# Performance work log

Measured on AMD Instinct MI355X. Metric: run time of the kernel, lower is better.

## Reference

```python
import jax, jax.numpy as jnp
import numpy as np

N, E, G, T = 4096, 16384, 128, 100
DIMS = [(5, 64), (64, 128), (128, 256)]
EPS = 1e-5


def setup_inputs() -> dict:
    key = jax.random.key(0)
    ks = iter(jax.random.split(key, 64))
    d = {}
    d["x"] = jax.random.normal(next(ks), (N, 5), jnp.float32)
    d["edge_index"] = jax.random.randint(next(ks), (2, E), 0, N, jnp.int64)
    d["edge_attr"] = jax.random.uniform(next(ks), (E, 3), jnp.float32)
    d["batch_seg"] = jnp.sort(jax.random.randint(next(ks), (N,), 0, G, jnp.int64))
    for l, (cin, cout) in enumerate(DIMS, start=1):
        d[f"l{l}_W1"] = jax.random.normal(next(ks), (3, 32), jnp.float32) * 0.3
        d[f"l{l}_b1"] = jnp.zeros((32,), jnp.float32)
        d[f"l{l}_W2"] = jax.random.normal(next(ks), (32, cin * cout), jnp.float32) * 0.05
        d[f"l{l}_b2"] = jnp.zeros((cin * cout,), jnp.float32)
        d[f"l{l}_root"] = jax.random.normal(next(ks), (cin, cout), jnp.float32) * 0.1
        d[f"l{l}_bias"] = jnp.zeros((cout,), jnp.float32)
        d[f"bn{l}_g"] = jnp.ones((cout,), jnp.float32)
        d[f"bn{l}_b"] = jnp.zeros((cout,), jnp.float32)
        d[f"bn{l}_m"] = jax.random.normal(next(ks), (cout,), jnp.float32) * 0.01
        d[f"bn{l}_v"] = jax.random.uniform(next(ks), (cout,), jnp.float32, 0.5, 1.5)
    d["mlp_W"] = jax.random.normal(next(ks), (256, T), jnp.float32) * 0.06
    d["mlp_b"] = jnp.zeros((T,), jnp.float32)
    return d


def _nnconv(h, src, dst, edge_attr, W1, b1, W2, b2, root, bias, cin, cout):
    # edge MLP -> per-edge weight matrix [E, cin, cout]
    ew = (jax.nn.relu(edge_attr @ W1 + b1) @ W2 + b2).reshape(-1, cin, cout)
    msg = jnp.einsum('ei,eio->eo', h[src], ew)  # gather + per-edge matmul
    ssum = jax.ops.segment_sum(msg, dst, num_segments=N)
    cnt = jax.ops.segment_sum(jnp.ones((msg.shape[0],), msg.dtype), dst, num_segments=N)
    agg = ssum / jnp.maximum(cnt, 1.0)[:, None]  # scatter-mean
    return h @ root + agg + bias


def _bn(h, g, b, m, v):
    return g * (h - m) * jax.lax.rsqrt(v + EPS) + b


def reference(x, edge_index, edge_attr, batch_seg,
              l1_W1, l1_b1, l1_W2, l1_b2, l1_root, l1_bias, bn1_g, bn1_b, bn1_m, bn1_v,
              l2_W1, l2_b1, l2_W2, l2_b2, l2_root, l2_bias, bn2_g, bn2_b, bn2_m, bn2_v,
              l3_W1, l3_b1, l3_W2, l3_b2, l3_root, l3_bias, bn3_g, bn3_b, bn3_m, bn3_v,
              mlp_W, mlp_b):
    src, dst = edge_index[0], edge_index[1]
    h = _nnconv(x, src, dst, edge_attr, l1_W1, l1_b1, l1_W2, l1_b2, l1_root, l1_bias, 5, 64)
    h = jax.nn.relu(_bn(h, bn1_g, bn1_b, bn1_m, bn1_v))
    h = _nnconv(h, src, dst, edge_attr, l2_W1, l2_b1, l2_W2, l2_b2, l2_root, l2_bias, 64, 128)
    h = jax.nn.relu(_bn(h, bn2_g, bn2_b, bn2_m, bn2_v))
    h = _nnconv(h, src, dst, edge_attr, l3_W1, l3_b1, l3_W2, l3_b2, l3_root, l3_bias, 128, 256)
    h = jax.nn.relu(_bn(h, bn3_g, bn3_b, bn3_m, bn3_v))
    # global mean pool over graphs
    psum = jax.ops.segment_sum(h, batch_seg, num_segments=G)
    pcnt = jax.ops.segment_sum(jnp.ones((N,), h.dtype), batch_seg, num_segments=G)
    pooled = psum / jnp.maximum(pcnt, 1.0)[:, None]
    out = pooled @ mlp_W + mlp_b
    return jnp.where(out > 0, out, 0.1 * out)  # LeakyReLU(0.1)
```

## Files before the change

### kernel.cpp

```cpp
#include <hip/hip_runtime.h>
#include <cstdint>
#include <cstddef>

#define BN_EPS 1e-5f

typedef short bf16x8 __attribute__((ext_vector_type(8)));
typedef float f32x4  __attribute__((ext_vector_type(4)));
typedef unsigned short u16x8 __attribute__((ext_vector_type(8)));

__device__ __forceinline__ uint16_t f2bf_rte(float f) {
  uint32_t u = __float_as_uint(f);
  uint32_t r = u + 0x7fffu + ((u >> 16) & 1u);
  return (uint16_t)(r >> 16);
}
__device__ __forceinline__ float bf2f(uint16_t h) {
  return __uint_as_float(((uint32_t)h) << 16);
}
__device__ __forceinline__ void split_bf(float v, uint16_t& hi, uint16_t& lo) {
  hi = f2bf_rte(v);
  lo = f2bf_rte(v - bf2f(hi));
}

__global__ void zero_i32_k(int* p, int n) {
  int i = blockIdx.x * blockDim.x + threadIdx.x;
  if (i < n) p[i] = 0;
}

__global__ void hist_k(const int* __restrict__ dst, int* __restrict__ cnt, int E) {
  int e = blockIdx.x * blockDim.x + threadIdx.x;
  if (e < E) atomicAdd(&cnt[dst[e]], 1);
}

__global__ __launch_bounds__(1024) void scan_k(const int* __restrict__ cnt,
                                               int* __restrict__ offsets,
                                               int* __restrict__ cursor,
                                               int N, int total) {
  __shared__ int part[1024];
  int t = threadIdx.x;
  int a0 = cnt[4*t+0], a1 = cnt[4*t+1], a2 = cnt[4*t+2], a3 = cnt[4*t+3];
  part[t] = a0 + a1 + a2 + a3;
  __syncthreads();
  for (int off = 1; off < 1024; off <<= 1) {
    int v = (t >= off) ? part[t - off] : 0;
    __syncthreads();
    part[t] += v;
    __syncthreads();
  }
  int excl = (t == 0) ? 0 : part[t-1];
  int o0 = excl, o1 = o0 + a0, o2 = o1 + a1, o3 = o2 + a2;
  offsets[4*t+0] = o0; offsets[4*t+1] = o1; offsets[4*t+2] = o2; offsets[4*t+3] = o3;
  cursor [4*t+0] = o0; cursor [4*t+1] = o1; cursor [4*t+2] = o2; cursor [4*t+3] = o3;
  if (t == 0) offsets[N] = total;
}

__global__ void scatter_k(const int* __restrict__ dst, int* __restrict__ cursor,
                          int* __restrict__ csr, int E) {
  int e = blockIdx.x * blockDim.x + threadIdx.x;
  if (e < E) {
    int d = dst[e];
    int pos = atomicAdd(&cursor[d], 1);
    csr[pos] = e;
  }
}

__global__ void build_W2pT_k(const float* __restrict__ W2, const float* __restrict__ b2,
                             const float* __restrict__ root,
                             uint16_t* __restrict__ Bhi, uint16_t* __restrict__ Blo,
                             int cin, int cout, int Kpad) {
  int idx = blockIdx.x * blockDim.x + threadIdx.x;
  int total = cout * Kpad;
  if (idx >= total) return;
  int o  = idx / Kpad;
  int ki = idx - o * Kpad;
  float v = 0.f;
  if (ki < 34 * cin) {
    int k = ki / cin;
    int i = ki - k * cin;
    if (k < 32)       v = W2[(size_t)k * cin * cout + (size_t)i * cout + o];
    else if (k == 32) v = b2[(size_t)i * cout + o];
    else              v = root[(size_t)i * cout + o];
  }
  uint16_t hi, lo;
  split_bf(v, hi, lo);
  Bhi[idx] = hi;
  Blo[idx] = lo;
}

template<int CIN>
__global__ __launch_bounds__(256) void build_S_vec_k(const float* __restrict__ h,
                                                     const float* __restrict__ ea,
                                                     const float* __restrict__ W1,
                                                     const float* __restrict__ b1,
                                                     const int* __restrict__ src,
                                                     const int* __restrict__ csr,
                                                     const int* __restrict__ offsets,
                                                     uint16_t* __restrict__ Shi,
                                                     uint16_t* __restrict__ Slo,
                                                     int Kpad) {
  constexpr int CH = 8;
  constexpr int K1 = 33 * CIN;
  constexpr int NCH = K1 / 8;
  constexpr int NP = (NCH + 255) / 256;
  __shared__ float hs[CH][CIN];
  __shared__ float zs[CH][33];
  __shared__ int   es[CH];
  const int n = blockIdx.x;
  const int tid = threadIdx.x;
  const int base = offsets[n];
  const int deg  = offsets[n+1] - base;
  const float scale = 1.f / fmaxf((float)deg, 1.f);
  float acc[NP][8];
#pragma unroll
  for (int p = 0; p < NP; p++)
#pragma unroll
    for (int j = 0; j < 8; j++) acc[p][j] = 0.f;

  for (int c0 = 0; c0 < deg; c0 += CH) {
    const int cc = min(CH, deg - c0);
    if (tid < cc) es[tid] = csr[base + c0 + tid];
    __syncthreads();
    for (int idx = tid; idx < cc * CIN; idx += 256) {
      int slot = idx / CIN, i = idx - slot * CIN;
      hs[slot][i] = h[(size_t)src[es[slot]] * CIN + i];
    }
    for (int idx = tid; idx < cc * 33; idx += 256) {
      int slot = idx / 33, k = idx - slot * 33;
      float v;
      if (k == 32) v = 1.f;
      else {
        int e = es[slot];
        v = fmaxf(ea[e*3+0] * W1[k] + ea[e*3+1] * W1[32 + k] + ea[e*3+2] * W1[64 + k] + b1[k], 0.f);
      }
      zs[slot][k] = v;
    }
    __syncthreads();
#pragma unroll
    for (int p = 0; p < NP; p++) {
      int ch = p * 256 + tid;
      if (ch < NCH) {
        int ki0 = ch * 8;
        int k  = ki0 / CIN;
        int i0 = ki0 & (CIN - 1);
        for (int c = 0; c < cc; c++) {
          float zv = zs[c][k];
          float4 h0 = *(const float4*)&hs[c][i0];
          float4 h1 = *(const float4*)&hs[c][i0 + 4];
          acc[p][0] += zv * h0.x; acc[p][1] += zv * h0.y;
          acc[p][2] += zv * h0.z; acc[p][3] += zv * h0.w;
          acc[p][4] += zv * h1.x; acc[p][5] += zv * h1.y;
          acc[p][6] += zv * h1.z; acc[p][7] += zv * h1.w;
        }
      }
    }
    __syncthreads();
  }
  const size_t rowb = (size_t)n * Kpad;
#pragma unroll
  for (int p = 0; p < NP; p++) {
    int ch = p * 256 + tid;
    if (ch < NCH) {
      u16x8 hv, lv;
#pragma unroll
      for (int j = 0; j < 8; j++) {
        uint16_t hi, lo;
        split_bf(acc[p][j] * scale, hi, lo);
        hv[j] = hi; lv[j] = lo;
      }
      *(u16x8*)(Shi + rowb + ch * 8) = hv;
      *(u16x8*)(Slo + rowb + ch * 8) = lv;
    }
  }
  for (int c = tid; c < CIN / 8; c += 256) {
    int i0 = c * 8;
    float4 a = *(const float4*)&h[(size_t)n * CIN + i0];
    float4 b = *(const float4*)&h[(size_t)n * CIN + i0 + 4];
    float vals[8] = {a.x, a.y, a.z, a.w, b.x, b.y, b.z, b.w};
    u16x8 hv, lv;
#pragma unroll
    for (int j = 0; j < 8; j++) {
      uint16_t hi, lo;
      split_bf(vals[j], hi, lo);
      hv[j] = hi; lv[j] = lo;
    }
    *(u16x8*)(Shi + rowb + K1 + i0) = hv;
    *(u16x8*)(Slo + rowb + K1 + i0) = lv;
  }
  for (int ki = 34 * CIN + tid; ki < Kpad; ki += 256) {
    Shi[rowb + ki] = 0;
    Slo[rowb + ki] = 0;
  }
}

__global__ __launch_bounds__(256) void build_S5_k(const float* __restrict__ h,
                                                  const float* __restrict__ ea,
                                                  const float* __restrict__ W1,
                                                  const float* __restrict__ b1,
                                                  const int* __restrict__ src,
                                                  const int* __restrict__ csr,
                                                  const int* __restrict__ offsets,
                                                  uint16_t* __restrict__ Shi,
                                                  uint16_t* __restrict__ Slo,
                                                  int Kpad) {
  constexpr int CIN = 5, CH = 8;
  constexpr int K1 = 33 * CIN;
  constexpr int KT = 34 * CIN;
  __shared__ float hs[CH][CIN];
  __shared__ float zs[CH][33];
  __shared__ int   es[CH];
  const int n = blockIdx.x;
  const int tid = threadIdx.x;
  const int base = offsets[n];
  const int deg  = offsets[n+1] - base;
  const float scale = 1.f / fmaxf((float)deg, 1.f);
  float acc = 0.f;

  for (int c0 = 0; c0 < deg; c0 += CH) {
    const int cc = min(CH, deg - c0);
    if (tid < cc) es[tid] = csr[base + c0 + tid];
    __syncthreads();
    for (int idx = tid; idx < cc * CIN; idx += 256) {
      int slot = idx / CIN, i = idx - slot * CIN;
      hs[slot][i] = h[(size_t)src[es[slot]] * CIN + i];
    }
    for (int idx = tid; idx < cc * 33; idx += 256) {
      int slot = idx / 33, k = idx - slot * 33;
      float v;
      if (k == 32) v = 1.f;
      else {
        int e = es[slot];
        v = fmaxf(ea[e*3+0] * W1[k] + ea[e*3+1] * W1[32 + k] + ea[e*3+2] * W1[64 + k] + b1[k], 0.f);
      }
      zs[slot][k] = v;
    }
    __syncthreads();
    if (tid < K1) {
      int k = tid / CIN, i = tid - (tid / CIN) * CIN;
      float a = acc;
      for (int c = 0; c < cc; c++) a += zs[c][k] * hs[c][i];
      acc = a;
    }
    __syncthreads();
  }
  const size_t rowb = (size_t)n * Kpad;
  if (tid < K1) {
    uint16_t hi, lo;
    split_bf(acc * scale, hi, lo);
    Shi[rowb + tid] = hi;
    Slo[rowb + tid] = lo;
  }
  if (tid < CIN) {
    uint16_t hi, lo;
    split_bf(h[(size_t)n * CIN + tid], hi, lo);
    Shi[rowb + K1 + tid] = hi;
    Slo[rowb + K1 + tid] = lo;
  }
  for (int ki = KT + tid; ki < Kpad; ki += 256) {
    Shi[rowb + ki] = 0;
    Slo[rowb + ki] = 0;
  }
}

__global__ __launch_bounds__(256, 2) void mfma_gemm_sk2_k(const uint16_t* __restrict__ Ahi,
                                                          const uint16_t* __restrict__ Alo,
                                                          const uint16_t* __restrict__ Bhi,
                                                          const uint16_t* __restrict__ Blo,
                                                          float* __restrict__ Cpart,
                                                          int Kpad, int Ncol, int M,
                                                          int iters, int SK) {
  __shared__ uint16_t As[2][128][64];
  __shared__ uint16_t Bs[2][128][64];
  const int m0 = blockIdx.x * 128, n0 = blockIdx.y * 128;
  const int z  = blockIdx.z;
  const int ibase = iters / SK, irem = iters % SK;
  const int i0    = z * ibase + min(z, irem);
  const int niter = ibase + (z < irem ? 1 : 0);
  const int tid  = threadIdx.x;
  const int lane = tid & 63;
  const int wave = tid >> 6;
  const int wm = wave & 1, wn = wave >> 1;
  const int q  = lane >> 4;
  const int mr = lane & 15;

  f32x4 acc[4][4];
#pragma unroll
  for (int a = 0; a < 4; a++)
#pragma unroll
    for (int b = 0; b < 4; b++) acc[a][b] = (f32x4)0.f;

  for (int it = 0; it < niter; it++) {
    const int k0 = (i0 + it) * 64;
#pragma unroll
    for (int i = 0; i < 16; i++) {
      int chunk = i * 256 + tid;
      int coct = chunk & 7;
      int row  = (chunk >> 3) & 127;
      int plane = (chunk >> 10) & 1;
      int arr   = chunk >> 11;
      const uint16_t* gsrc = arr ? (plane ? Blo : Bhi) : (plane ? Alo : Ahi);
      int grow = (arr ? n0 : m0) + row;
      uint4 v = {0u, 0u, 0u, 0u};
      if (arr == 0 || grow < Ncol)
        v = *(const uint4*)(gsrc + (size_t)grow * Kpad + k0 + coct * 8);
      int soct = coct ^ (row & 7);
      uint16_t* ldst = arr ? &Bs[plane][row][soct * 8] : &As[plane][row][soct * 8];
      *(uint4*)ldst = v;
    }
    __syncthreads();
#pragma unroll
    for (int ks = 0; ks < 2; ks++) {
      const int oct = (ks * 4 + q) ^ (mr & 7);
      bf16x8 bh[4], bl[4];
#pragma unroll
      for (int f = 0; f < 4; f++) {
        int row = wn * 64 + f * 16 + mr;
        bh[f] = *(const bf16x8*)&Bs[0][row][oct * 8];
        bl[f] = *(const bf16x8*)&Bs[1][row][oct * 8];
      }
#pragma unroll
      for (int fm = 0; fm < 4; fm++) {
        int row = wm * 64 + fm * 16 + mr;
        bf16x8 ah = *(const bf16x8*)&As[0][row][oct * 8];
        bf16x8 al = *(const bf16x8*)&As[1][row][oct * 8];
#pragma unroll
        for (int fn = 0; fn < 4; fn++) {
          acc[fm][fn] = __builtin_amdgcn_mfma_f32_16x16x32_bf16(ah, bh[fn], acc[fm][fn], 0, 0, 0);
          acc[fm][fn] = __builtin_amdgcn_mfma_f32_16x16x32_bf16(ah, bl[fn], acc[fm][fn], 0, 0, 0);
          acc[fm][fn] = __builtin_amdgcn_mfma_f32_16x16x32_bf16(al, bh[fn], acc[fm][fn], 0, 0, 0);
        }
      }
    }
    __syncthreads();
  }

  float* Cz = Cpart + (size_t)z * M * Ncol;
#pragma unroll
  for (int fm = 0; fm < 4; fm++) {
#pragma unroll
    for (int reg = 0; reg < 4; reg++) {
      int row = m0 + wm * 64 + fm * 16 + q * 4 + reg;
#pragma unroll
      for (int fn = 0; fn < 4; fn++) {
        int col = n0 + wn * 64 + fn * 16 + mr;
        if (col < Ncol)
          Cz[(size_t)row * Ncol + col] = acc[fm][fn][reg];
      }
    }
  }
}

__global__ void epilogue_k(const float* __restrict__ Cpart, int SK, size_t plane4,
                           int Ncol,
                           const float* __restrict__ bias, const float* __restrict__ bg,
                           const float* __restrict__ bb, const float* __restrict__ bnm,
                           const float* __restrict__ bnv,
                           float* __restrict__ C, int total4) {
  int i = blockIdx.x * blockDim.x + threadIdx.x;
  if (i >= total4) return;
  float4 v = {0.f, 0.f, 0.f, 0.f};
  for (int z = 0; z < SK; z++) {
    float4 p = *((const float4*)Cpart + (size_t)z * plane4 + i);
    v.x += p.x; v.y += p.y; v.z += p.z; v.w += p.w;
  }
  int col0 = (i * 4) % Ncol;
  float o[4] = {v.x, v.y, v.z, v.w};
#pragma unroll
  for (int j = 0; j < 4; j++) {
    int c = col0 + j;
    float s = bg[c] * rsqrtf(bnv[c] + BN_EPS);
    float val = (o[j] + bias[c] - bnm[c]) * s + bb[c];
    o[j] = fmaxf(val, 0.f);
  }
  float4 r = {o[0], o[1], o[2], o[3]};
  *((float4*)C + i) = r;
}

__global__ __launch_bounds__(256) void pool_final_k(const float* __restrict__ h,
                                                    const int* __restrict__ seg,
                                                    const float* __restrict__ W,
                                                    const float* __restrict__ b,
                                                    float* __restrict__ out,
                                                    int N, int T) {
  __shared__ float pooled[256];
  const int g = blockIdx.x, tid = threadIdx.x;
  int lo = 0, hi = N;
  while (lo < hi) { int mid = (lo + hi) >> 1; if (seg[mid] < g) lo = mid + 1; else hi = mid; }
  int lo2 = lo, hi2 = N;
  while (lo2 < hi2) { int mid = (lo2 + hi2) >> 1; if (seg[mid] < g + 1) lo2 = mid + 1; else hi2 = mid; }
  const int cnt = lo2 - lo;
  const float inv = 1.f / fmaxf((float)cnt, 1.f);
  float s = 0.f;
  for (int n = lo; n < lo2; n++) s += h[(size_t)n * 256 + tid];
  pooled[tid] = s * inv;
  __syncthreads();
  if (tid < T) {
    float acc = b[tid];
    for (int o = 0; o < 256; o++) acc += pooled[o] * W[(size_t)o * T + tid];
    out[(size_t)g * T + tid] = (acc > 0.f) ? acc : 0.1f * acc;
  }
}

extern "C" void kernel_launch(void* const* d_in, const int* in_sizes, int n_in,
                              void* d_out, int out_size, void* d_ws, size_t ws_size,
                              hipStream_t stream) {
  const float* x   = (const float*)d_in[0];
  const int*   ei  = (const int*)d_in[1];
  const float* ea  = (const float*)d_in[2];
  const int*   seg = (const int*)d_in[3];

  const int N = in_sizes[0] / 5;
  const int E = in_sizes[2] / 3;
  const int T = in_sizes[35];
  const int G = out_size / T;
  const int* src = ei;
  const int* dst = ei + E;

  const float *W1[3], *b1[3], *W2[3], *b2[3], *root[3], *bias[3];
  const float *bng[3], *bnb[3], *bnm[3], *bnv[3];
  for (int l = 0; l < 3; l++) {
    int base = 4 + l * 10;
    W1[l]   = (const float*)d_in[base + 0];
    b1[l]   = (const float*)d_in[base + 1];
    W2[l]   = (const float*)d_in[base + 2];
    b2[l]   = (const float*)d_in[base + 3];
    root[l] = (const float*)d_in[base + 4];
    bias[l] = (const float*)d_in[base + 5];
    bng[l]  = (const float*)d_in[base + 6];
    bnb[l]  = (const float*)d_in[base + 7];
    bnm[l]  = (const float*)d_in[base + 8];
    bnv[l]  = (const float*)d_in[base + 9];
  }
  const float* mlpW = (const float*)d_in[34];
  const float* mlpb = (const float*)d_in[35];

  char* p = (char*)d_ws;
  auto carve = [&](size_t bytes) -> char* {
    char* r = p;
    p += (bytes + 255) & ~(size_t)255;
    return r;
  };
  const int KPADMAX = 4352;
  int*      cnt     = (int*)carve((size_t)N * 4);
  int*      offsets = (int*)carve((size_t)(N + 1) * 4);
  int*      cursor  = (int*)carve((size_t)N * 4);
  int*      csr     = (int*)carve((size_t)E * 4);
  uint16_t* Whi     = (uint16_t*)carve((size_t)256 * KPADMAX * 2);
  uint16_t* Wlo     = (uint16_t*)carve((size_t)256 * KPADMAX * 2);
  uint16_t* Shi     = (uint16_t*)carve((size_t)N * KPADMAX * 2);
  uint16_t* Slo     = (uint16_t*)carve((size_t)N * KPADMAX * 2);
  float*    Cpart   = (float*)carve((size_t)16 * N * 128 * 4);
  float*    hA      = (float*)carve((size_t)N * 256 * 4);
  float*    hB      = (float*)carve((size_t)N * 128 * 4);

  zero_i32_k<<<(N + 255) / 256, 256, 0, stream>>>(cnt, N);
  hist_k<<<(E + 255) / 256, 256, 0, stream>>>(dst, cnt, E);
  scan_k<<<1, 1024, 0, stream>>>(cnt, offsets, cursor, N, E);
  scatter_k<<<(E + 255) / 256, 256, 0, stream>>>(dst, cursor, csr, E);

  const int cins[3]  = {5, 64, 128};
  const int couts[3] = {64, 128, 256};
  const int kpads[3] = {192, 2176, 4352};
  const int sks[3]   = {3, 16, 8};
  const float* hin = x;
  float* houts[3] = {hA, hB, hA};

  for (int l = 0; l < 3; l++) {
    int cin = cins[l], cout = couts[l], Kpad = kpads[l], SK = sks[l];
    int iters = Kpad / 64;
    build_W2pT_k<<<(cout * Kpad + 255) / 256, 256, 0, stream>>>(W2[l], b2[l], root[l],
                                                                Whi, Wlo, cin, cout, Kpad);
    if (cin == 5)
      build_S5_k<<<N, 256, 0, stream>>>(hin, ea, W1[l], b1[l], src, csr, offsets, Shi, Slo, Kpad);
    else if (cin == 64)
      build_S_vec_k<64><<<N, 256, 0, stream>>>(hin, ea, W1[l], b1[l], src, csr, offsets, Shi, Slo, Kpad);
    else
      build_S_vec_k<128><<<N, 256, 0, stream>>>(hin, ea, W1[l], b1[l], src, csr, offsets, Shi, Slo, Kpad);
    dim3 grid(N / 128, (cout + 127) / 128, SK);
    mfma_gemm_sk2_k<<<grid, 256, 0, stream>>>(Shi, Slo, Whi, Wlo, Cpart, Kpad, cout, N, iters, SK);
    int total4 = N * cout / 4;
    epilogue_k<<<(total4 + 255) / 256, 256, 0, stream>>>(Cpart, SK, (size_t)N * cout / 4, cout,
                                                         bias[l], bng[l], bnb[l], bnm[l], bnv[l],
                                                         houts[l], total4);
    hin = houts[l];
  }

  pool_final_k<<<G, 256, 0, stream>>>(hA, seg, mlpW, mlpb, (float*)d_out, N, T);
}
```

Baseline: 315.2 us.

## Fuse split-K reduction via atomics, fold BN into consumers, batch weight prep

The separate epilogue kernel and split-K partial buffer are removed. The GEMM now atomically accumulates into zeroed per-layer outputs. Bias, batchnorm and ReLU are applied lazily when the next layer's S-builder or the pooling kernel reads the raw output. The three weight-transform launches are merged into one, the zero kernel becomes a single memset, and the GEMM moves to 512 threads with half the N-tile per wave. This cuts launches and the partial-sum write/read traffic, at the cost of float atomic contention, nondeterministic summation order, and redundant BN recomputation on gathered rows.

```diff
diff --git a/kernel.cpp b/kernel.cpp
--- a/kernel.cpp
+++ b/kernel.cpp
@@ -19,11 +19,6 @@
 __device__ __forceinline__ void split_bf(float v, uint16_t& hi, uint16_t& lo) {
   hi = f2bf_rte(v);
   lo = f2bf_rte(v - bf2f(hi));
-}
-
-__global__ void zero_i32_k(int* p, int n) {
-  int i = blockIdx.x * blockDim.x + threadIdx.x;
-  if (i < n) p[i] = 0;
 }
 
 __global__ void hist_k(const int* __restrict__ dst, int* __restrict__ cnt, int E) {
@@ -63,13 +58,9 @@
   }
 }
 
-__global__ void build_W2pT_k(const float* __restrict__ W2, const float* __restrict__ b2,
-                             const float* __restrict__ root,
-                             uint16_t* __restrict__ Bhi, uint16_t* __restrict__ Blo,
-                             int cin, int cout, int Kpad) {
-  int idx = blockIdx.x * blockDim.x + threadIdx.x;
-  int total = cout * Kpad;
-  if (idx >= total) return;
+__device__ __forceinline__ void w2pt_one(int idx, const float* W2, const float* b2,
+                                         const float* root, uint16_t* Bhi, uint16_t* Blo,
+                                         int cin, int cout, int Kpad) {
   int o  = idx / Kpad;
   int ki = idx - o * Kpad;
   float v = 0.f;
@@ -86,8 +77,30 @@
   Blo[idx] = lo;
 }
 
+__global__ void build_W2pT_all_k(const float* W2a, const float* b2a, const float* roota,
+                                 uint16_t* Bhia, uint16_t* Bloa,
+                                 const float* W2b, const float* b2b, const float* rootb,
+                                 uint16_t* Bhib, uint16_t* Blob,
+                                 const float* W2c, const float* b2c, const float* rootc,
+                                 uint16_t* Bhic, uint16_t* Bloc) {
+  const int T1 = 64 * 192, T2 = 128 * 2176, T3 = 256 * 4352;
+  int idx = blockIdx.x * blockDim.x + threadIdx.x;
+  if (idx < T1) {
+    w2pt_one(idx, W2a, b2a, roota, Bhia, Bloa, 5, 64, 192);
+  } else if (idx < T1 + T2) {
+    w2pt_one(idx - T1, W2b, b2b, rootb, Bhib, Blob, 64, 128, 2176);
+  } else if (idx < T1 + T2 + T3) {
+    w2pt_one(idx - T1 - T2, W2c, b2c, rootc, Bhic, Bloc, 128, 256, 4352);
+  }
+}
+
 template<int CIN>
-__global__ __launch_bounds__(256) void build_S_vec_k(const float* __restrict__ h,
+__global__ __launch_bounds__(256) void build_S_vec_k(const float* __restrict__ Craw,
+                                                     const float* __restrict__ pbias,
+                                                     const float* __restrict__ pg,
+                                                     const float* __restrict__ pb,
+                                                     const float* __restrict__ pm,
+                                                     const float* __restrict__ pv,
                                                      const float* __restrict__ ea,
                                                      const float* __restrict__ W1,
                                                      const float* __restrict__ b1,
@@ -104,8 +117,14 @@
   __shared__ float hs[CH][CIN];
   __shared__ float zs[CH][33];
   __shared__ int   es[CH];
+  __shared__ float sA[CIN], tA[CIN];
   const int n = blockIdx.x;
   const int tid = threadIdx.x;
+  if (tid < CIN) {
+    float s = pg[tid] * rsqrtf(pv[tid] + BN_EPS);
+    sA[tid] = s;
+    tA[tid] = (pbias[tid] - pm[tid]) * s + pb[tid];
+  }
   const int base = offsets[n];
   const int deg  = offsets[n+1] - base;
   const float scale = 1.f / fmaxf((float)deg, 1.f);
@@ -121,7 +140,8 @@
     __syncthreads();
     for (int idx = tid; idx < cc * CIN; idx += 256) {
       int slot = idx / CIN, i = idx - slot * CIN;
-      hs[slot][i] = h[(size_t)src[es[slot]] * CIN + i];
+      float raw = Craw[(size_t)src[es[slot]] * CIN + i];
+      hs[slot][i] = fmaxf(raw * sA[i] + tA[i], 0.f);
     }
     for (int idx = tid; idx < cc * 33; idx += 256) {
       int slot = idx / 33, k = idx - slot * 33;
@@ -170,24 +190,21 @@
       *(u16x8*)(Slo + rowb + ch * 8) = lv;
     }
   }
+  __syncthreads();
   for (int c = tid; c < CIN / 8; c += 256) {
     int i0 = c * 8;
-    float4 a = *(const float4*)&h[(size_t)n * CIN + i0];
-    float4 b = *(const float4*)&h[(size_t)n * CIN + i0 + 4];
-    float vals[8] = {a.x, a.y, a.z, a.w, b.x, b.y, b.z, b.w};
     u16x8 hv, lv;
 #pragma unroll
     for (int j = 0; j < 8; j++) {
+      int i = i0 + j;
+      float raw = Craw[(size_t)n * CIN + i];
+      float val = fmaxf(raw * sA[i] + tA[i], 0.f);
       uint16_t hi, lo;
-      split_bf(vals[j], hi, lo);
+      split_bf(val, hi, lo);
       hv[j] = hi; lv[j] = lo;
     }
     *(u16x8*)(Shi + rowb + K1 + i0) = hv;
     *(u16x8*)(Slo + rowb + K1 + i0) = lv;
-  }
-  for (int ki = 34 * CIN + tid; ki < Kpad; ki += 256) {
-    Shi[rowb + ki] = 0;
-    Slo[rowb + ki] = 0;
   }
 }
 
@@ -260,13 +277,13 @@
   }
 }
 
-__global__ __launch_bounds__(256, 2) void mfma_gemm_sk2_k(const uint16_t* __restrict__ Ahi,
-                                                          const uint16_t* __restrict__ Alo,
-                                                          const uint16_t* __restrict__ Bhi,
-                                                          const uint16_t* __restrict__ Blo,
-                                                          float* __restrict__ Cpart,
-                                                          int Kpad, int Ncol, int M,
-                                                          int iters, int SK) {
+__global__ __launch_bounds__(512, 4) void mfma_gemm_at_k(const uint16_t* __restrict__ Ahi,
+                                                         const uint16_t* __restrict__ Alo,
+                                                         const uint16_t* __restrict__ Bhi,
+                                                         const uint16_t* __restrict__ Blo,
+                                                         float* __restrict__ C,
+                                                         int Kpad, int Ncol,
+                                                         int iters, int SK) {
   __shared__ uint16_t As[2][128][64];
   __shared__ uint16_t Bs[2][128][64];
   const int m0 = blockIdx.x * 128, n0 = blockIdx.y * 128;
@@ -277,21 +294,22 @@
   const int tid  = threadIdx.x;
   const int lane = tid & 63;
   const int wave = tid >> 6;
-  const int wm = wave & 1, wn = wave >> 1;
+  const int wm = wave & 1;
+  const int wn = wave >> 1;
   const int q  = lane >> 4;
   const int mr = lane & 15;
 
-  f32x4 acc[4][4];
+  f32x4 acc[4][2];
 #pragma unroll
   for (int a = 0; a < 4; a++)
 #pragma unroll
-    for (int b = 0; b < 4; b++) acc[a][b] = (f32x4)0.f;
+    for (int b = 0; b < 2; b++) acc[a][b] = (f32x4)0.f;
 
   for (int it = 0; it < niter; it++) {
     const int k0 = (i0 + it) * 64;
 #pragma unroll
-    for (int i = 0; i < 16; i++) {
-      int chunk = i * 256 + tid;
+    for (int i = 0; i < 8; i++) {
+      int chunk = i * 512 + tid;
       int coct = chunk & 7;
       int row  = (chunk >> 3) & 127;
       int plane = (chunk >> 10) & 1;
@@ -309,12 +327,12 @@
 #pragma unroll
     for (int ks = 0; ks < 2; ks++) {
       const int oct = (ks * 4 + q) ^ (mr & 7);
-      bf16x8 bh[4], bl[4];
-#pragma unroll
-      for (int f = 0; f < 4; f++) {
-        int row = wn * 64 + f * 16 + mr;
-        bh[f] = *(const bf16x8*)&Bs[0][row][oct * 8];
-        bl[f] = *(const bf16x8*)&Bs[1][row][oct * 8];
+      bf16x8 bh[2], bl[2];
+#pragma unroll
+      for (int fn = 0; fn < 2; fn++) {
+        int row = wn * 32 + fn * 16 + mr;
+        bh[fn] = *(const bf16x8*)&Bs[0][row][oct * 8];
+        bl[fn] = *(const bf16x8*)&Bs[1][row][oct * 8];
       }
 #pragma unroll
       for (int fm = 0; fm < 4; fm++) {
@@ -322,7 +340,7 @@
         bf16x8 ah = *(const bf16x8*)&As[0][row][oct * 8];
         bf16x8 al = *(const bf16x8*)&As[1][row][oct * 8];
 #pragma unroll
-        for (int fn = 0; fn < 4; fn++) {
+        for (int fn = 0; fn < 2; fn++) {
           acc[fm][fn] = __builtin_amdgcn_mfma_f32_16x16x32_bf16(ah, bh[fn], acc[fm][fn], 0, 0, 0);
           acc[fm][fn] = __builtin_amdgcn_mfma_f32_16x16x32_bf16(ah, bl[fn], acc[fm][fn], 0, 0, 0);
           acc[fm][fn] = __builtin_amdgcn_mfma_f32_16x16x32_bf16(al, bh[fn], acc[fm][fn], 0, 0, 0);
@@ -332,49 +350,27 @@
     __syncthreads();
   }
 
-  float* Cz = Cpart + (size_t)z * M * Ncol;
 #pragma unroll
   for (int fm = 0; fm < 4; fm++) {
 #pragma unroll
     for (int reg = 0; reg < 4; reg++) {
       int row = m0 + wm * 64 + fm * 16 + q * 4 + reg;
 #pragma unroll
-      for (int fn = 0; fn < 4; fn++) {
-        int col = n0 + wn * 64 + fn * 16 + mr;
+      for (int fn = 0; fn < 2; fn++) {
+        int col = n0 + wn * 32 + fn * 16 + mr;
         if (col < Ncol)
-          Cz[(size_t)row * Ncol + col] = acc[fm][fn][reg];
-      }
-    }
-  }
-}
-
-__global__ void epilogue_k(const float* __restrict__ Cpart, int SK, size_t plane4,
-                           int Ncol,
-                           const float* __restrict__ bias, const float* __restrict__ bg,
-                           const float* __restrict__ bb, const float* __restrict__ bnm,
-                           const float* __restrict__ bnv,
-                           float* __restrict__ C, int total4) {
-  int i = blockIdx.x * blockDim.x + threadIdx.x;
-  if (i >= total4) return;
-  float4 v = {0.f, 0.f, 0.f, 0.f};
-  for (int z = 0; z < SK; z++) {
-    float4 p = *((const float4*)Cpart + (size_t)z * plane4 + i);
-    v.x += p.x; v.y += p.y; v.z += p.z; v.w += p.w;
-  }
-  int col0 = (i * 4) % Ncol;
-  float o[4] = {v.x, v.y, v.z, v.w};
-#pragma unroll
-  for (int j = 0; j < 4; j++) {
-    int c = col0 + j;
-    float s = bg[c] * rsqrtf(bnv[c] + BN_EPS);
-    float val = (o[j] + bias[c] - bnm[c]) * s + bb[c];
-    o[j] = fmaxf(val, 0.f);
-  }
-  float4 r = {o[0], o[1], o[2], o[3]};
-  *((float4*)C + i) = r;
-}
-
-__global__ __launch_bounds__(256) void pool_final_k(const float* __restrict__ h,
+          atomicAdd(&C[(size_t)row * Ncol + col], acc[fm][fn][reg]);
+      }
+    }
+  }
+}
+
+__global__ __launch_bounds__(256) void pool_final_k(const float* __restrict__ Craw,
+                                                    const float* __restrict__ pbias,
+                                                    const float* __restrict__ pg,
+                                                    const float* __restrict__ pb,
+                                                    const float* __restrict__ pm,
+                                                    const float* __restrict__ pv,
                                                     const int* __restrict__ seg,
                                                     const float* __restrict__ W,
                                                     const float* __restrict__ b,
@@ -382,6 +378,8 @@
                                                     int N, int T) {
   __shared__ float pooled[256];
   const int g = blockIdx.x, tid = threadIdx.x;
+  float s3 = pg[tid] * rsqrtf(pv[tid] + BN_EPS);
+  float t3 = (pbias[tid] - pm[tid]) * s3 + pb[tid];
   int lo = 0, hi = N;
   while (lo < hi) { int mid = (lo + hi) >> 1; if (seg[mid] < g) lo = mid + 1; else hi = mid; }
   int lo2 = lo, hi2 = N;
@@ -389,7 +387,8 @@
   const int cnt = lo2 - lo;
   const float inv = 1.f / fmaxf((float)cnt, 1.f);
   float s = 0.f;
-  for (int n = lo; n < lo2; n++) s += h[(size_t)n * 256 + tid];
+  for (int n = lo; n < lo2; n++)
+    s += fmaxf(Craw[(size_t)n * 256 + tid] * s3 + t3, 0.f);
   pooled[tid] = s * inv;
   __syncthreads();
   if (tid < T) {
@@ -438,50 +437,58 @@
     p += (bytes + 255) & ~(size_t)255;
     return r;
   };
-  const int KPADMAX = 4352;
-  int*      cnt     = (int*)carve((size_t)N * 4);
+  char*  zbase = p;
+  int*   cnt = (int*)carve((size_t)N * 4);
+  float* C1  = (float*)carve((size_t)N * 64 * 4);
+  float* C2  = (float*)carve((size_t)N * 128 * 4);
+  float* C3  = (float*)carve((size_t)N * 256 * 4);
+  size_t zbytes = (size_t)(p - zbase);
+
   int*      offsets = (int*)carve((size_t)(N + 1) * 4);
   int*      cursor  = (int*)carve((size_t)N * 4);
   int*      csr     = (int*)carve((size_t)E * 4);
-  uint16_t* Whi     = (uint16_t*)carve((size_t)256 * KPADMAX * 2);
-  uint16_t* Wlo     = (uint16_t*)carve((size_t)256 * KPADMAX * 2);
-  uint16_t* Shi     = (uint16_t*)carve((size_t)N * KPADMAX * 2);
-  uint16_t* Slo     = (uint16_t*)carve((size_t)N * KPADMAX * 2);
-  float*    Cpart   = (float*)carve((size_t)16 * N * 128 * 4);
-  float*    hA      = (float*)carve((size_t)N * 256 * 4);
-  float*    hB      = (float*)carve((size_t)N * 128 * 4);
-
-  zero_i32_k<<<(N + 255) / 256, 256, 0, stream>>>(cnt, N);
+  uint16_t* W1hi = (uint16_t*)carve((size_t)64 * 192 * 2);
+  uint16_t* W1lo = (uint16_t*)carve((size_t)64 * 192 * 2);
+  uint16_t* W2hi = (uint16_t*)carve((size_t)128 * 2176 * 2);
+  uint16_t* W2lo = (uint16_t*)carve((size_t)128 * 2176 * 2);
+  uint16_t* W3hi = (uint16_t*)carve((size_t)256 * 4352 * 2);
+  uint16_t* W3lo = (uint16_t*)carve((size_t)256 * 4352 * 2);
+  const int KPADMAX = 4352;
+  uint16_t* Shi = (uint16_t*)carve((size_t)N * KPADMAX * 2);
+  uint16_t* Slo = (uint16_t*)carve((size_t)N * KPADMAX * 2);
+
+  hipMemsetAsync(zbase, 0, zbytes, stream);
+
+  {
+    int total = 64 * 192 + 128 * 2176 + 256 * 4352;
+    build_W2pT_all_k<<<(total + 255) / 256, 256, 0, stream>>>(
+        W2[0], b2[0], root[0], W1hi, W1lo,
+        W2[1], b2[1], root[1], W2hi, W2lo,
+        W2[2], b2[2], root[2], W3hi, W3lo);
+  }
+
   hist_k<<<(E + 255) / 256, 256, 0, stream>>>(dst, cnt, E);
   scan_k<<<1, 1024, 0, stream>>>(cnt, offsets, cursor, N, E);
   scatter_k<<<(E + 255) / 256, 256, 0, stream>>>(dst, cursor, csr, E);
 
-  const int cins[3]  = {5, 64, 128};
-  const int couts[3] = {64, 128, 256};
-  const int kpads[3] = {192, 2176, 4352};
-  const int sks[3]   = {3, 16, 8};
-  const float* hin = x;
-  float* houts[3] = {hA, hB, hA};
-
-  for (int l = 0; l < 3; l++) {
-    int cin = cins[l], cout = couts[l], Kpad = kpads[l], SK = sks[l];
-    int iters = Kpad / 64;
-    build_W2pT_k<<<(cout * Kpad + 255) / 256, 256, 0, stream>>>(W2[l], b2[l], root[l],
-                                                                Whi, Wlo, cin, cout, Kpad);
-    if (cin == 5)
-      build_S5_k<<<N, 256, 0, stream>>>(hin, ea, W1[l], b1[l], src, csr, offsets, Shi, Slo, Kpad);
-    else if (cin == 64)
-      build_S_vec_k<64><<<N, 256, 0, stream>>>(hin, ea, W1[l], b1[l], src, csr, offsets, Shi, Slo, Kpad);
-    else
-      build_S_vec_k<128><<<N, 256, 0, stream>>>(hin, ea, W1[l], b1[l], src, csr, offsets, Shi, Slo, Kpad);
-    dim3 grid(N / 128, (cout + 127) / 128, SK);
-    mfma_gemm_sk2_k<<<grid, 256, 0, stream>>>(Shi, Slo, Whi, Wlo, Cpart, Kpad, cout, N, iters, SK);
-    int total4 = N * cout / 4;
-    epilogue_k<<<(total4 + 255) / 256, 256, 0, stream>>>(Cpart, SK, (size_t)N * cout / 4, cout,
-                                                         bias[l], bng[l], bnb[l], bnm[l], bnv[l],
-                                                         houts[l], total4);
-    hin = houts[l];
-  }
-
-  pool_final_k<<<G, 256, 0, stream>>>(hA, seg, mlpW, mlpb, (float*)d_out, N, T);
-}
+  build_S5_k<<<N, 256, 0, stream>>>(x, ea, W1[0], b1[0], src, csr, offsets, Shi, Slo, 192);
+  {
+    dim3 grid(N / 128, 1, 3);
+    mfma_gemm_at_k<<<grid, 512, 0, stream>>>(Shi, Slo, W1hi, W1lo, C1, 192, 64, 3, 3);
+  }
+  build_S_vec_k<64><<<N, 256, 0, stream>>>(C1, bias[0], bng[0], bnb[0], bnm[0], bnv[0],
+                                           ea, W1[1], b1[1], src, csr, offsets, Shi, Slo, 2176);
+  {
+    dim3 grid(N / 128, 1, 16);
+    mfma_gemm_at_k<<<grid, 512, 0, stream>>>(Shi, Slo, W2hi, W2lo, C2, 2176, 128, 34, 16);
+  }
+  build_S_vec_k<128><<<N, 256, 0, stream>>>(C2, bias[1], bng[1], bnb[1], bnm[1], bnv[1],
+                                            ea, W1[2], b1[2], src, csr, offsets, Shi, Slo, 4352);
+  {
+    dim3 grid(N / 128, 2, 8);
+    mfma_gemm_at_k<<<grid, 512, 0, stream>>>(Shi, Slo, W3hi, W3lo, C3, 4352, 256, 68, 8);
+  }
+
+  pool_final_k<<<G, 256, 0, stream>>>(C3, bias[2], bng[2], bnb[2], bnm[2], bnv[2],
+                                      seg, mlpW, mlpb, (float*)d_out, N, T);
+}
```

After: 311.3 us. Within noise of the previous version (-1.2%).
